# Kernel optimization log

Measured on AMD Instinct MI355X. Metric: run time of the kernel, lower is better.

## Reference

```python
import jax, jax.numpy as jnp
import numpy as np

DIM = 512
HID = 4 * DIM
E = 8
B, T = 2, 2048


def setup_inputs() -> dict:
    key = jax.random.key(0)
    ks = jax.random.split(key, 8)
    s = 0.02
    x = jax.random.normal(ks[0], (B, T, DIM), dtype=jnp.float32)
    route = jax.random.randint(ks[1], (B * T,), 0, E, dtype=jnp.int32)
    # stacked per-expert params; Linear y = x @ W + b with W in [in, out] layout
    w_in = jax.random.normal(ks[2], (E, DIM, HID), dtype=jnp.float32) * s
    b_in = jnp.zeros((E, HID), dtype=jnp.float32)
    w_gate = jax.random.normal(ks[3], (E, DIM, HID), dtype=jnp.float32) * s
    b_gate = jnp.zeros((E, HID), dtype=jnp.float32)
    w_out = jax.random.normal(ks[4], (E, HID, DIM), dtype=jnp.float32) * s
    b_out = jnp.zeros((E, DIM), dtype=jnp.float32)
    return {"x": x, "route": route, "w_in": w_in, "b_in": b_in,
            "w_gate": w_gate, "b_gate": b_gate, "w_out": w_out, "b_out": b_out}


def reference(x, route, w_in, b_in, w_gate, b_gate, w_out, b_out):
    Bb, Tt, C = x.shape
    xf = x.reshape(-1, C)  # [N, C]
    out = jnp.zeros_like(xf)
    n_experts = w_in.shape[0]
    # loop over the small fixed expert set; each expert is a SwiGLU FFN,
    # output scattered back by masking (same math as output[idx] += expert(x[idx]))
    for e in range(n_experts):
        mask = (route == e).astype(xf.dtype)[:, None]  # [N, 1]
        h = jax.nn.silu(xf @ w_gate[e] + b_gate[e]) * (xf @ w_in[e] + b_in[e])  # [N, 4C]
        out = out + mask * (h @ w_out[e] + b_out[e])
    return out.reshape(Bb, Tt, C)
```

## Files before the change

kernel.cpp:

```cpp
#include <hip/hip_runtime.h>

#define DIM 512
#define HID 2048
#define NEXP 8

typedef __attribute__((ext_vector_type(8))) short v8s;
typedef __attribute__((ext_vector_type(4))) float v4f;

__device__ __forceinline__ unsigned short f2bf(float f) {
  union { __bf16 b; unsigned short u; } c;
  c.b = (__bf16)f;
  return c.u;
}

__device__ __forceinline__ void gload16(const void* g, void* l) {
  __builtin_amdgcn_global_load_lds(
      (const __attribute__((address_space(1))) unsigned int*)g,
      (__attribute__((address_space(3))) unsigned int*)l, 16, 0, 0);
}

__global__ void route_prep(const int* __restrict__ route, int* __restrict__ meta, int ntok) {
  __shared__ int c[NEXP];
  int t = threadIdx.x;
  if (t < NEXP) c[t] = 0;
  __syncthreads();
  for (int n = t; n < ntok; n += blockDim.x) atomicAdd(&c[route[n]], 1);
  __syncthreads();
  if (t == 0) {
    int acc = 0, pacc = 0;
    for (int e = 0; e < NEXP; ++e) {
      meta[e] = c[e];
      meta[NEXP + e] = acc;
      meta[2 * NEXP + e] = acc;
      meta[3 * NEXP + e] = pacc;
      acc += c[e];
      pacc += ((c[e] + 127) >> 7) << 7;
    }
  }
}

__global__ void fill_perm(const int* __restrict__ route, int* __restrict__ meta,
                          int* __restrict__ perm, int ntok) {
  int n = blockIdx.x * blockDim.x + threadIdx.x;
  if (n < ntok) {
    int p = atomicAdd(&meta[2 * NEXP + route[n]], 1);
    perm[p] = n;
  }
}

__global__ __launch_bounds__(256) void x_conv(
    const float* __restrict__ x, const int* __restrict__ meta,
    const int* __restrict__ perm, unsigned short* __restrict__ xp)
{
  const int bid = blockIdx.x;
  const int e = bid & 7;
  const int mt = bid >> 3;
  const int cnt = meta[e];
  const int padded = ((cnt + 127) >> 7) << 7;
  if (mt * 64 >= padded) return;
  const int off  = meta[NEXP + e];
  const int poff = meta[3 * NEXP + e];
  const int t = threadIdx.x;
  const int r = t & 63, q = t >> 6;
  int arow = mt * 64 + r; if (arow >= cnt) arow = cnt - 1;
  const float* src = x + (size_t)perm[off + arow] * DIM + q * 128;
  unsigned short* dst = xp + (size_t)((poff + mt * 64) >> 6) * 32768;
  #pragma unroll
  for (int j = 0; j < 16; ++j) {
    float4 f0 = ((const float4*)src)[2 * j];
    float4 f1 = ((const float4*)src)[2 * j + 1];
    v8s v;
    v[0] = (short)f2bf(f0.x); v[1] = (short)f2bf(f0.y);
    v[2] = (short)f2bf(f0.z); v[3] = (short)f2bf(f0.w);
    v[4] = (short)f2bf(f1.x); v[5] = (short)f2bf(f1.y);
    v[6] = (short)f2bf(f1.z); v[7] = (short)f2bf(f1.w);
    *(v8s*)(dst + (size_t)((q * 16 + j) * 64 + r) * 8) = v;
  }
}

__global__ __launch_bounds__(256) void wgi_conv(
    const float* __restrict__ wg, const float* __restrict__ wi,
    unsigned short* __restrict__ wgp, unsigned short* __restrict__ wip)
{
  const int s = blockIdx.x;
  const int j = blockIdx.y;
  const int e = blockIdx.z >> 1;
  const int which = blockIdx.z & 1;
  const float* src = (which ? wi : wg) + (size_t)e * DIM * HID;
  unsigned short* dst = (which ? wip : wgp) + (((size_t)e * 16 + j) * 8 + s) * 8192;
  const int t = threadIdx.x;
  #pragma unroll
  for (int i = 0; i < 4; ++i) {
    const int c = t + 256 * i;
    const int kq = c >> 7, n = c & 127;
    const float* srow = src + (size_t)(s * 64 + kq * 8) * HID + j * 128 + n;
    v8s r;
    #pragma unroll
    for (int q = 0; q < 8; ++q) r[q] = (short)f2bf(srow[(size_t)q * HID]);
    *(v8s*)(dst + (size_t)c * 8) = r;
  }
}

__global__ __launch_bounds__(256) void wo_conv(
    const float* __restrict__ wo, unsigned short* __restrict__ wop)
{
  const int s = blockIdx.x;
  const int j = blockIdx.y;
  const int e = blockIdx.z;
  const float* src = wo + (size_t)e * HID * DIM;
  unsigned short* dst = wop + (((size_t)e * 8 + j) * 32 + s) * 4096;
  const int t = threadIdx.x;
  #pragma unroll
  for (int i = 0; i < 2; ++i) {
    const int c = t + 256 * i;
    const int kq = c >> 6, n = c & 63;
    const float* srow = src + (size_t)(s * 64 + kq * 8) * DIM + j * 64 + n;
    v8s r;
    #pragma unroll
    for (int q = 0; q < 8; ++q) r[q] = (short)f2bf(srow[(size_t)q * DIM]);
    *(v8s*)(dst + (size_t)c * 8) = r;
  }
}

__global__ __launch_bounds__(256, 4) void gemm1g(
    const unsigned short* __restrict__ xp,
    const unsigned short* __restrict__ wgp, const float* __restrict__ bg_,
    const unsigned short* __restrict__ wip, const float* __restrict__ bi_,
    const int* __restrict__ meta,
    unsigned short* __restrict__ hbuf)
{
  const int bid = blockIdx.x;
  const int stripe = bid & 255;
  const int mt = bid >> 8;
  const int e = stripe >> 5, j = stripe & 31;
  const int cnt = meta[e];
  const int m0 = mt * 128;
  if (m0 >= cnt) return;
  const int poff = meta[3 * NEXP + e];
  const int n0 = j * 64;

  __shared__ __align__(16) unsigned char lds[32768];

  const int t = threadIdx.x;
  const int l = t & 63, w = t >> 6;
  const int wm = w >> 1, wn = w & 1;
  const int fr = l & 15, fg = l >> 4;

  const int tile0 = (poff + m0) >> 6;
  const int half = j & 1;
  const unsigned short* pg = wgp + ((size_t)e * 16 + (j >> 1)) * 65536;
  const unsigned short* pi = wip + ((size_t)e * 16 + (j >> 1)) * 65536;

  const int aq0 = t >> 7, am0 = t & 127;
  const int aq1 = (t + 256) >> 7, am1 = t & 127;
  const int gq = t >> 6, gn = t & 63;

  v4f aG[4][2], aI[4][2];
  #pragma unroll
  for (int i = 0; i < 4; ++i)
    #pragma unroll
    for (int q = 0; q < 2; ++q) {
      aG[i][q] = (v4f){0.f, 0.f, 0.f, 0.f};
      aI[i][q] = (v4f){0.f, 0.f, 0.f, 0.f};
    }

  auto stage = [&](int s, int b) {
    unsigned char* base = lds + b * 16384;
    gload16(xp + (size_t)(tile0 + (am0 >> 6)) * 32768 + ((size_t)(s * 4 + aq0) * 64 + (am0 & 63)) * 8,
            base + t * 16);
    gload16(xp + (size_t)(tile0 + (am1 >> 6)) * 32768 + ((size_t)(s * 4 + aq1) * 64 + (am1 & 63)) * 8,
            base + (t + 256) * 16);
    const size_t woff = (size_t)(s >> 1) * 8192 + ((size_t)((s & 1) * 4 + gq) * 128 + half * 64 + gn) * 8;
    gload16(pg + woff, base + 8192 + t * 16);
    gload16(pi + woff, base + 12288 + t * 16);
  };

  stage(0, 0);
  __syncthreads();

  int cur = 0;
  for (int s = 0; s < 16; ++s) {
    if (s < 15) stage(s + 1, cur ^ 1);
    const unsigned char* base = lds + cur * 16384;
    v8s af[4], gf[2], inf[2];
    #pragma unroll
    for (int mf = 0; mf < 4; ++mf)
      af[mf] = *(const v8s*)(base + (fg * 128 + wm * 64 + mf * 16 + fr) * 16);
    #pragma unroll
    for (int nf = 0; nf < 2; ++nf) {
      gf[nf]  = *(const v8s*)(base + 8192  + (fg * 64 + wn * 32 + nf * 16 + fr) * 16);
      inf[nf] = *(const v8s*)(base + 12288 + (fg * 64 + wn * 32 + nf * 16 + fr) * 16);
    }
    #pragma unroll
    for (int mf = 0; mf < 4; ++mf)
      #pragma unroll
      for (int nf = 0; nf < 2; ++nf) {
        aG[mf][nf] = __builtin_amdgcn_mfma_f32_16x16x32_bf16(af[mf], gf[nf],  aG[mf][nf], 0, 0, 0);
        aI[mf][nf] = __builtin_amdgcn_mfma_f32_16x16x32_bf16(af[mf], inf[nf], aI[mf][nf], 0, 0, 0);
      }
    __syncthreads();
    cur ^= 1;
  }

  #pragma unroll
  for (int nf = 0; nf < 2; ++nf) {
    const int c = n0 + wn * 32 + nf * 16 + fr;
    const float bg = bg_[(size_t)e * HID + c];
    const float bi = bi_[(size_t)e * HID + c];
    #pragma unroll
    for (int mf = 0; mf < 4; ++mf)
      #pragma unroll
      for (int jj = 0; jj < 4; ++jj) {
        const int r = wm * 64 + mf * 16 + fg * 4 + jj;
        const float g = aG[mf][nf][jj] + bg;
        const float v = aI[mf][nf][jj] + bi;
        const float hval = g / (1.f + __expf(-g)) * v;
        const int grow = poff + m0 + r;
        hbuf[(size_t)(grow >> 6) * 131072 + ((size_t)(c >> 3) * 64 + (grow & 63)) * 8 + (c & 7)] = f2bf(hval);
      }
  }
}

__global__ __launch_bounds__(256, 4) void gemm2g(
    const unsigned short* __restrict__ hbuf,
    const unsigned short* __restrict__ wop, const float* __restrict__ bo_,
    const int* __restrict__ meta, const int* __restrict__ perm,
    float* __restrict__ out)
{
  const int bid = blockIdx.x;
  const int stripe = bid & 63;
  const int mt = bid >> 6;
  const int e = stripe >> 3, jn = stripe & 7;
  const int cnt = meta[e];
  const int m0 = mt * 64;
  if (m0 >= cnt) return;
  const int off = meta[NEXP + e], poff = meta[3 * NEXP + e];
  const int n0 = jn * 64;

  __shared__ __align__(16) unsigned char lds[32768];

  const int t = threadIdx.x;
  const int l = t & 63, w = t >> 6;
  const int wm = w >> 1, wn = w & 1;
  const int fr = l & 15, fg = l >> 4;

  const unsigned short* pa = hbuf + (size_t)((poff + m0) >> 6) * 131072;
  const unsigned short* pb = wop + ((size_t)e * 8 + jn) * 131072;

  v4f acc[2][2];
  #pragma unroll
  for (int i = 0; i < 2; ++i) {
    acc[i][0] = (v4f){0.f, 0.f, 0.f, 0.f};
    acc[i][1] = (v4f){0.f, 0.f, 0.f, 0.f};
  }

  auto stage = [&](int s, int b) {
    unsigned char* base = lds + b * 16384;
    #pragma unroll
    for (int i = 0; i < 2; ++i) {
      const int c = t + 256 * i;
      gload16(pa + (size_t)s * 4096 + (size_t)c * 8, base + c * 16);
    }
    #pragma unroll
    for (int i = 0; i < 2; ++i) {
      const int c = t + 256 * i;
      gload16(pb + (size_t)s * 4096 + (size_t)c * 8, base + 8192 + c * 16);
    }
  };

  stage(0, 0);
  __syncthreads();

  int cur = 0;
  for (int s = 0; s < 32; ++s) {
    if (s < 31) stage(s + 1, cur ^ 1);
    const unsigned char* base = lds + cur * 16384;
    #pragma unroll
    for (int kk = 0; kk < 2; ++kk) {
      v8s af[2], bf[2];
      #pragma unroll
      for (int mf = 0; mf < 2; ++mf)
        af[mf] = *(const v8s*)(base + ((kk * 4 + fg) * 64 + wm * 32 + mf * 16 + fr) * 16);
      #pragma unroll
      for (int nf = 0; nf < 2; ++nf)
        bf[nf] = *(const v8s*)(base + 8192 + ((kk * 4 + fg) * 64 + wn * 32 + nf * 16 + fr) * 16);
      #pragma unroll
      for (int mf = 0; mf < 2; ++mf)
        #pragma unroll
        for (int nf = 0; nf < 2; ++nf)
          acc[mf][nf] = __builtin_amdgcn_mfma_f32_16x16x32_bf16(af[mf], bf[nf], acc[mf][nf], 0, 0, 0);
    }
    __syncthreads();
    cur ^= 1;
  }

  #pragma unroll
  for (int nf = 0; nf < 2; ++nf) {
    const int c = n0 + wn * 32 + nf * 16 + fr;
    const float bo = bo_[(size_t)e * DIM + c];
    #pragma unroll
    for (int mf = 0; mf < 2; ++mf)
      #pragma unroll
      for (int jj = 0; jj < 4; ++jj) {
        const int r = wm * 32 + mf * 16 + fg * 4 + jj;
        if (m0 + r < cnt)
          out[(size_t)perm[off + m0 + r] * DIM + c] = acc[mf][nf][jj] + bo;
      }
  }
}

extern "C" void kernel_launch(void* const* d_in, const int* in_sizes, int n_in,
                              void* d_out, int out_size, void* d_ws, size_t ws_size,
                              hipStream_t stream) {
  const float* x      = (const float*)d_in[0];
  const int*   route  = (const int*)d_in[1];
  const float* w_in   = (const float*)d_in[2];
  const float* b_in   = (const float*)d_in[3];
  const float* w_gate = (const float*)d_in[4];
  const float* b_gate = (const float*)d_in[5];
  const float* w_out  = (const float*)d_in[6];
  const float* b_out  = (const float*)d_in[7];
  float* out = (float*)d_out;

  const int ntok = in_sizes[1];

  int* meta = (int*)d_ws;
  int* perm = (int*)((char*)d_ws + 128);

  const size_t W_OFF  = 65536;
  const size_t WMAT   = (size_t)NEXP * DIM * HID * 2;
  unsigned short* wgp  = (unsigned short*)((char*)d_ws + W_OFF);
  unsigned short* wip  = (unsigned short*)((char*)d_ws + W_OFF + WMAT);
  unsigned short* wop  = wgp;
  unsigned short* xp   = (unsigned short*)((char*)d_ws + W_OFF + 2 * WMAT);
  unsigned short* hbuf = (unsigned short*)((char*)d_ws + W_OFF + 2 * WMAT + 5242880);

  const int MT64  = (ntok + 63) / 64;
  const int MT128 = (ntok + 127) / 128;

  route_prep<<<1, 256, 0, stream>>>(route, meta, ntok);
  fill_perm<<<(ntok + 255) / 256, 256, 0, stream>>>(route, meta, perm, ntok);
  x_conv<<<NEXP * MT64, 256, 0, stream>>>(x, meta, perm, xp);
  wgi_conv<<<dim3(8, 16, 16), 256, 0, stream>>>(w_gate, w_in, wgp, wip);
  gemm1g<<<256 * MT128, 256, 0, stream>>>(
      xp, wgp, b_gate, wip, b_in, meta, hbuf);
  wo_conv<<<dim3(32, 8, 8), 256, 0, stream>>>(w_out, wop);
  gemm2g<<<64 * MT64, 256, 0, stream>>>(
      hbuf, wop, b_out, meta, perm, out);
}
```

Before: 119.5 us.

## Triple-buffer LDS in both expert GEMMs with explicit vmcnt waits and barriers

Both grouped GEMM kernels move from double-buffered to triple-buffered LDS staging with a prefetch distance of two k-steps. The __syncthreads calls are replaced by explicit s_waitcnt vmcnt counters and raw s_barrier, with sched_barrier fences so the compiler keeps the order. This is meant to hide more global-to-LDS load latency behind the MFMA work. In exchange, LDS per block grows to 48KB and launch bounds drop to 3 blocks per CU, which lowers occupancy, and the hand-set vmcnt values are fragile if the number of loads per stage changes.

```diff
diff --git a/kernel.cpp b/kernel.cpp
--- a/kernel.cpp
+++ b/kernel.cpp
@@ -122,7 +122,7 @@
   }
 }
 
-__global__ __launch_bounds__(256, 4) void gemm1g(
+__global__ __launch_bounds__(256, 3) void gemm1t(
     const unsigned short* __restrict__ xp,
     const unsigned short* __restrict__ wgp, const float* __restrict__ bg_,
     const unsigned short* __restrict__ wip, const float* __restrict__ bi_,
@@ -139,7 +139,7 @@
   const int poff = meta[3 * NEXP + e];
   const int n0 = j * 64;
 
-  __shared__ __align__(16) unsigned char lds[32768];
+  __shared__ __align__(16) unsigned char lds[49152];
 
   const int t = threadIdx.x;
   const int l = t & 63, w = t >> 6;
@@ -152,7 +152,6 @@
   const unsigned short* pi = wip + ((size_t)e * 16 + (j >> 1)) * 65536;
 
   const int aq0 = t >> 7, am0 = t & 127;
-  const int aq1 = (t + 256) >> 7, am1 = t & 127;
   const int gq = t >> 6, gn = t & 63;
 
   v4f aG[4][2], aI[4][2];
@@ -168,7 +167,7 @@
     unsigned char* base = lds + b * 16384;
     gload16(xp + (size_t)(tile0 + (am0 >> 6)) * 32768 + ((size_t)(s * 4 + aq0) * 64 + (am0 & 63)) * 8,
             base + t * 16);
-    gload16(xp + (size_t)(tile0 + (am1 >> 6)) * 32768 + ((size_t)(s * 4 + aq1) * 64 + (am1 & 63)) * 8,
+    gload16(xp + (size_t)(tile0 + (am0 >> 6)) * 32768 + ((size_t)(s * 4 + aq0 + 2) * 64 + (am0 & 63)) * 8,
             base + (t + 256) * 16);
     const size_t woff = (size_t)(s >> 1) * 8192 + ((size_t)((s & 1) * 4 + gq) * 128 + half * 64 + gn) * 8;
     gload16(pg + woff, base + 8192 + t * 16);
@@ -176,12 +175,17 @@
   };
 
   stage(0, 0);
-  __syncthreads();
-
-  int cur = 0;
+  stage(1, 1);
+  __builtin_amdgcn_sched_barrier(0);
+  asm volatile("s_waitcnt vmcnt(4)" ::: "memory");
+  __builtin_amdgcn_sched_barrier(0);
+  __builtin_amdgcn_s_barrier();
+  __builtin_amdgcn_sched_barrier(0);
+
   for (int s = 0; s < 16; ++s) {
-    if (s < 15) stage(s + 1, cur ^ 1);
-    const unsigned char* base = lds + cur * 16384;
+    if (s + 2 < 16) stage(s + 2, (s + 2) % 3);
+    __builtin_amdgcn_sched_barrier(0);
+    const unsigned char* base = lds + (s % 3) * 16384;
     v8s af[4], gf[2], inf[2];
     #pragma unroll
     for (int mf = 0; mf < 4; ++mf)
@@ -198,8 +202,17 @@
         aG[mf][nf] = __builtin_amdgcn_mfma_f32_16x16x32_bf16(af[mf], gf[nf],  aG[mf][nf], 0, 0, 0);
         aI[mf][nf] = __builtin_amdgcn_mfma_f32_16x16x32_bf16(af[mf], inf[nf], aI[mf][nf], 0, 0, 0);
       }
-    __syncthreads();
-    cur ^= 1;
+    if (s < 15) {
+      __builtin_amdgcn_sched_barrier(0);
+      if (s + 2 < 16) {
+        asm volatile("s_waitcnt vmcnt(4)" ::: "memory");
+      } else {
+        asm volatile("s_waitcnt vmcnt(0)" ::: "memory");
+      }
+      __builtin_amdgcn_sched_barrier(0);
+      __builtin_amdgcn_s_barrier();
+      __builtin_amdgcn_sched_barrier(0);
+    }
   }
 
   #pragma unroll
@@ -221,7 +234,7 @@
   }
 }
 
-__global__ __launch_bounds__(256, 4) void gemm2g(
+__global__ __launch_bounds__(256, 3) void gemm2t(
     const unsigned short* __restrict__ hbuf,
     const unsigned short* __restrict__ wop, const float* __restrict__ bo_,
     const int* __restrict__ meta, const int* __restrict__ perm,
@@ -237,7 +250,7 @@
   const int off = meta[NEXP + e], poff = meta[3 * NEXP + e];
   const int n0 = jn * 64;
 
-  __shared__ __align__(16) unsigned char lds[32768];
+  __shared__ __align__(16) unsigned char lds[49152];
 
   const int t = threadIdx.x;
   const int l = t & 63, w = t >> 6;
@@ -260,21 +273,22 @@
     for (int i = 0; i < 2; ++i) {
       const int c = t + 256 * i;
       gload16(pa + (size_t)s * 4096 + (size_t)c * 8, base + c * 16);
-    }
-    #pragma unroll
-    for (int i = 0; i < 2; ++i) {
-      const int c = t + 256 * i;
       gload16(pb + (size_t)s * 4096 + (size_t)c * 8, base + 8192 + c * 16);
     }
   };
 
   stage(0, 0);
-  __syncthreads();
-
-  int cur = 0;
+  stage(1, 1);
+  __builtin_amdgcn_sched_barrier(0);
+  asm volatile("s_waitcnt vmcnt(4)" ::: "memory");
+  __builtin_amdgcn_sched_barrier(0);
+  __builtin_amdgcn_s_barrier();
+  __builtin_amdgcn_sched_barrier(0);
+
   for (int s = 0; s < 32; ++s) {
-    if (s < 31) stage(s + 1, cur ^ 1);
-    const unsigned char* base = lds + cur * 16384;
+    if (s + 2 < 32) stage(s + 2, (s + 2) % 3);
+    __builtin_amdgcn_sched_barrier(0);
+    const unsigned char* base = lds + (s % 3) * 16384;
     #pragma unroll
     for (int kk = 0; kk < 2; ++kk) {
       v8s af[2], bf[2];
@@ -290,8 +304,17 @@
         for (int nf = 0; nf < 2; ++nf)
           acc[mf][nf] = __builtin_amdgcn_mfma_f32_16x16x32_bf16(af[mf], bf[nf], acc[mf][nf], 0, 0, 0);
     }
-    __syncthreads();
-    cur ^= 1;
+    if (s < 31) {
+      __builtin_amdgcn_sched_barrier(0);
+      if (s + 2 < 32) {
+        asm volatile("s_waitcnt vmcnt(4)" ::: "memory");
+      } else {
+        asm volatile("s_waitcnt vmcnt(0)" ::: "memory");
+      }
+      __builtin_amdgcn_sched_barrier(0);
+      __builtin_amdgcn_s_barrier();
+      __builtin_amdgcn_sched_barrier(0);
+    }
   }
 
   #pragma unroll
@@ -342,9 +365,9 @@
   fill_perm<<<(ntok + 255) / 256, 256, 0, stream>>>(route, meta, perm, ntok);
   x_conv<<<NEXP * MT64, 256, 0, stream>>>(x, meta, perm, xp);
   wgi_conv<<<dim3(8, 16, 16), 256, 0, stream>>>(w_gate, w_in, wgp, wip);
-  gemm1g<<<256 * MT128, 256, 0, stream>>>(
+  gemm1t<<<256 * MT128, 256, 0, stream>>>(
       xp, wgp, b_gate, wip, b_in, meta, hbuf);
   wo_conv<<<dim3(32, 8, 8), 256, 0, stream>>>(w_out, wop);
-  gemm2g<<<64 * MT64, 256, 0, stream>>>(
+  gemm2t<<<64 * MT64, 256, 0, stream>>>(
       hbuf, wop, b_out, meta, perm, out);
 }
```

Result: no change. 121.1 us (+1.3%).

## Fuse gate/in weight bf16 conversion into weight-stationary GEMM1 over all M tiles

Applied to the files above, without the earlier changes.

Removes the separate wgi_conv pass and its bf16 workspace copy. GEMM1 now gives each block one expert and a 32-column slice, and the block converts the fp32 gate and in weights for that slice into LDS once. It keeps those weights resident while it loops over every 128-row token tile of the expert, streaming only activations through double-buffered LDS. This cuts weight traffic and a kernel launch, but uses 80KB LDS per block, fixes the grid at 512 blocks, and serializes the M tiles inside each block, so per-block work depends on how routing balances across experts.

```diff
diff --git a/kernel.cpp b/kernel.cpp
--- a/kernel.cpp
+++ b/kernel.cpp
@@ -78,29 +78,6 @@
   }
 }
 
-__global__ __launch_bounds__(256) void wgi_conv(
-    const float* __restrict__ wg, const float* __restrict__ wi,
-    unsigned short* __restrict__ wgp, unsigned short* __restrict__ wip)
-{
-  const int s = blockIdx.x;
-  const int j = blockIdx.y;
-  const int e = blockIdx.z >> 1;
-  const int which = blockIdx.z & 1;
-  const float* src = (which ? wi : wg) + (size_t)e * DIM * HID;
-  unsigned short* dst = (which ? wip : wgp) + (((size_t)e * 16 + j) * 8 + s) * 8192;
-  const int t = threadIdx.x;
-  #pragma unroll
-  for (int i = 0; i < 4; ++i) {
-    const int c = t + 256 * i;
-    const int kq = c >> 7, n = c & 127;
-    const float* srow = src + (size_t)(s * 64 + kq * 8) * HID + j * 128 + n;
-    v8s r;
-    #pragma unroll
-    for (int q = 0; q < 8; ++q) r[q] = (short)f2bf(srow[(size_t)q * HID]);
-    *(v8s*)(dst + (size_t)c * 8) = r;
-  }
-}
-
 __global__ __launch_bounds__(256) void wo_conv(
     const float* __restrict__ wo, unsigned short* __restrict__ wop)
 {
@@ -122,98 +99,111 @@
   }
 }
 
-__global__ __launch_bounds__(256, 4) void gemm1g(
+__global__ __launch_bounds__(256, 2) void gemm1w(
     const unsigned short* __restrict__ xp,
-    const unsigned short* __restrict__ wgp, const float* __restrict__ bg_,
-    const unsigned short* __restrict__ wip, const float* __restrict__ bi_,
+    const float* __restrict__ wg_, const float* __restrict__ bg_,
+    const float* __restrict__ wi_, const float* __restrict__ bi_,
     const int* __restrict__ meta,
     unsigned short* __restrict__ hbuf)
 {
   const int bid = blockIdx.x;
-  const int stripe = bid & 255;
-  const int mt = bid >> 8;
-  const int e = stripe >> 5, j = stripe & 31;
+  const int e = bid >> 6;
+  const int j = bid & 63;
   const int cnt = meta[e];
-  const int m0 = mt * 128;
-  if (m0 >= cnt) return;
   const int poff = meta[3 * NEXP + e];
-  const int n0 = j * 64;
-
-  __shared__ __align__(16) unsigned char lds[32768];
+  const int n0 = j * 32;
+
+  __shared__ __align__(16) unsigned char lds[81920];
 
   const int t = threadIdx.x;
   const int l = t & 63, w = t >> 6;
   const int wm = w >> 1, wn = w & 1;
   const int fr = l & 15, fg = l >> 4;
 
-  const int tile0 = (poff + m0) >> 6;
-  const int half = j & 1;
-  const unsigned short* pg = wgp + ((size_t)e * 16 + (j >> 1)) * 65536;
-  const unsigned short* pi = wip + ((size_t)e * 16 + (j >> 1)) * 65536;
-
-  const int aq0 = t >> 7, am0 = t & 127;
-  const int aq1 = (t + 256) >> 7, am1 = t & 127;
-  const int gq = t >> 6, gn = t & 63;
-
-  v4f aG[4][2], aI[4][2];
-  #pragma unroll
-  for (int i = 0; i < 4; ++i)
-    #pragma unroll
-    for (int q = 0; q < 2; ++q) {
-      aG[i][q] = (v4f){0.f, 0.f, 0.f, 0.f};
-      aI[i][q] = (v4f){0.f, 0.f, 0.f, 0.f};
-    }
-
-  auto stage = [&](int s, int b) {
-    unsigned char* base = lds + b * 16384;
-    gload16(xp + (size_t)(tile0 + (am0 >> 6)) * 32768 + ((size_t)(s * 4 + aq0) * 64 + (am0 & 63)) * 8,
-            base + t * 16);
-    gload16(xp + (size_t)(tile0 + (am1 >> 6)) * 32768 + ((size_t)(s * 4 + aq1) * 64 + (am1 & 63)) * 8,
-            base + (t + 256) * 16);
-    const size_t woff = (size_t)(s >> 1) * 8192 + ((size_t)((s & 1) * 4 + gq) * 128 + half * 64 + gn) * 8;
-    gload16(pg + woff, base + 8192 + t * 16);
-    gload16(pi + woff, base + 12288 + t * 16);
-  };
-
-  stage(0, 0);
-  __syncthreads();
-
-  int cur = 0;
-  for (int s = 0; s < 16; ++s) {
-    if (s < 15) stage(s + 1, cur ^ 1);
-    const unsigned char* base = lds + cur * 16384;
-    v8s af[4], gf[2], inf[2];
-    #pragma unroll
-    for (int mf = 0; mf < 4; ++mf)
-      af[mf] = *(const v8s*)(base + (fg * 128 + wm * 64 + mf * 16 + fr) * 16);
-    #pragma unroll
-    for (int nf = 0; nf < 2; ++nf) {
-      gf[nf]  = *(const v8s*)(base + 8192  + (fg * 64 + wn * 32 + nf * 16 + fr) * 16);
-      inf[nf] = *(const v8s*)(base + 12288 + (fg * 64 + wn * 32 + nf * 16 + fr) * 16);
-    }
-    #pragma unroll
-    for (int mf = 0; mf < 4; ++mf)
-      #pragma unroll
-      for (int nf = 0; nf < 2; ++nf) {
-        aG[mf][nf] = __builtin_amdgcn_mfma_f32_16x16x32_bf16(af[mf], gf[nf],  aG[mf][nf], 0, 0, 0);
-        aI[mf][nf] = __builtin_amdgcn_mfma_f32_16x16x32_bf16(af[mf], inf[nf], aI[mf][nf], 0, 0, 0);
-      }
+  {
+    const int r0 = t >> 1;
+    const int h  = t & 1;
+    #pragma unroll
+    for (int m = 0; m < 2; ++m) {
+      const float* src = (m ? wi_ : wg_) + (size_t)e * DIM * HID + n0 + h * 16;
+      unsigned char* slab = lds + m * 32768;
+      #pragma unroll
+      for (int p = 0; p < 4; ++p) {
+        const int r = p * 128 + r0;
+        const float* row = src + (size_t)r * HID;
+        float f[16];
+        #pragma unroll
+        for (int q = 0; q < 4; ++q) {
+          float4 v = ((const float4*)row)[q];
+          f[4*q] = v.x; f[4*q+1] = v.y; f[4*q+2] = v.z; f[4*q+3] = v.w;
+        }
+        unsigned char* dst = slab + ((r >> 3) * 32 + h * 16) * 16 + (r & 7) * 2;
+        #pragma unroll
+        for (int nn = 0; nn < 16; ++nn)
+          *(unsigned short*)(dst + nn * 16) = f2bf(f[nn]);
+      }
+    }
+  }
+
+  const int c = n0 + wn * 16 + fr;
+  const float bgv = bg_[(size_t)e * HID + c];
+  const float biv = bi_[(size_t)e * HID + c];
+
+  unsigned char* albuf = lds + 65536;
+  const int nmt = (cnt + 127) >> 7;
+
+  for (int mt = 0; mt < nmt; ++mt) {
+    const int m0 = mt * 128;
+    const int tile0 = (poff + m0) >> 6;
+
+    auto stage_a = [&](int s, int b) {
+      unsigned char* base = albuf + b * 8192;
+      #pragma unroll
+      for (int i = 0; i < 2; ++i) {
+        const int s_ = t + 256 * i;
+        const int kq = s_ >> 7, mr = s_ & 127;
+        gload16(xp + (size_t)(tile0 + (mr >> 6)) * 32768 +
+                     ((size_t)(s * 4 + kq) * 64 + (mr & 63)) * 8,
+                base + s_ * 16);
+      }
+    };
+
+    stage_a(0, 0);
     __syncthreads();
-    cur ^= 1;
-  }
-
-  #pragma unroll
-  for (int nf = 0; nf < 2; ++nf) {
-    const int c = n0 + wn * 32 + nf * 16 + fr;
-    const float bg = bg_[(size_t)e * HID + c];
-    const float bi = bi_[(size_t)e * HID + c];
+
+    v4f aG[4], aI[4];
+    #pragma unroll
+    for (int i = 0; i < 4; ++i) {
+      aG[i] = (v4f){0.f, 0.f, 0.f, 0.f};
+      aI[i] = (v4f){0.f, 0.f, 0.f, 0.f};
+    }
+
+    int cur = 0;
+    for (int s = 0; s < 16; ++s) {
+      if (s < 15) stage_a(s + 1, cur ^ 1);
+      const unsigned char* base = albuf + cur * 8192;
+      v8s af[4], gf, inf;
+      #pragma unroll
+      for (int mf = 0; mf < 4; ++mf)
+        af[mf] = *(const v8s*)(base + (fg * 128 + wm * 64 + mf * 16 + fr) * 16);
+      gf  = *(const v8s*)(lds + (((s * 4 + fg) * 32) + wn * 16 + fr) * 16);
+      inf = *(const v8s*)(lds + 32768 + (((s * 4 + fg) * 32) + wn * 16 + fr) * 16);
+      #pragma unroll
+      for (int mf = 0; mf < 4; ++mf) {
+        aG[mf] = __builtin_amdgcn_mfma_f32_16x16x32_bf16(af[mf], gf,  aG[mf], 0, 0, 0);
+        aI[mf] = __builtin_amdgcn_mfma_f32_16x16x32_bf16(af[mf], inf, aI[mf], 0, 0, 0);
+      }
+      __syncthreads();
+      cur ^= 1;
+    }
+
     #pragma unroll
     for (int mf = 0; mf < 4; ++mf)
       #pragma unroll
       for (int jj = 0; jj < 4; ++jj) {
         const int r = wm * 64 + mf * 16 + fg * 4 + jj;
-        const float g = aG[mf][nf][jj] + bg;
-        const float v = aI[mf][nf][jj] + bi;
+        const float g = aG[mf][jj] + bgv;
+        const float v = aI[mf][jj] + biv;
         const float hval = g / (1.f + __expf(-g)) * v;
         const int grow = poff + m0 + r;
         hbuf[(size_t)(grow >> 6) * 131072 + ((size_t)(c >> 3) * 64 + (grow & 63)) * 8 + (c & 7)] = f2bf(hval);
@@ -260,10 +250,6 @@
     for (int i = 0; i < 2; ++i) {
       const int c = t + 256 * i;
       gload16(pa + (size_t)s * 4096 + (size_t)c * 8, base + c * 16);
-    }
-    #pragma unroll
-    for (int i = 0; i < 2; ++i) {
-      const int c = t + 256 * i;
       gload16(pb + (size_t)s * 4096 + (size_t)c * 8, base + 8192 + c * 16);
     }
   };
@@ -327,23 +313,17 @@
   int* meta = (int*)d_ws;
   int* perm = (int*)((char*)d_ws + 128);
 
-  const size_t W_OFF  = 65536;
-  const size_t WMAT   = (size_t)NEXP * DIM * HID * 2;
-  unsigned short* wgp  = (unsigned short*)((char*)d_ws + W_OFF);
-  unsigned short* wip  = (unsigned short*)((char*)d_ws + W_OFF + WMAT);
-  unsigned short* wop  = wgp;
-  unsigned short* xp   = (unsigned short*)((char*)d_ws + W_OFF + 2 * WMAT);
-  unsigned short* hbuf = (unsigned short*)((char*)d_ws + W_OFF + 2 * WMAT + 5242880);
-
-  const int MT64  = (ntok + 63) / 64;
-  const int MT128 = (ntok + 127) / 128;
+  unsigned short* xp   = (unsigned short*)((char*)d_ws + 65536);
+  unsigned short* wop  = (unsigned short*)((char*)d_ws + 65536 + 5242880);
+  unsigned short* hbuf = (unsigned short*)((char*)d_ws + 65536 + 5242880 + 16777216);
+
+  const int MT64 = (ntok + 63) / 64;
 
   route_prep<<<1, 256, 0, stream>>>(route, meta, ntok);
   fill_perm<<<(ntok + 255) / 256, 256, 0, stream>>>(route, meta, perm, ntok);
   x_conv<<<NEXP * MT64, 256, 0, stream>>>(x, meta, perm, xp);
-  wgi_conv<<<dim3(8, 16, 16), 256, 0, stream>>>(w_gate, w_in, wgp, wip);
-  gemm1g<<<256 * MT128, 256, 0, stream>>>(
-      xp, wgp, b_gate, wip, b_in, meta, hbuf);
+  gemm1w<<<NEXP * 64, 256, 0, stream>>>(
+      xp, w_gate, b_gate, w_in, b_in, meta, hbuf);
   wo_conv<<<dim3(32, 8, 8), 256, 0, stream>>>(w_out, wop);
   gemm2g<<<64 * MT64, 256, 0, stream>>>(
       hbuf, wop, b_out, meta, perm, out);
```

Result: faster. 114.0 us (-4.6%).
